# Performance work log

Measured on AMD Instinct MI355X. Metric: run time of the kernel, lower is better.

The kernel has to match this reference:

```python
import jax, jax.numpy as jnp
import numpy as np

B, L, D, H, S, E, FF = 4, 2048, 1024, 16, 512, 8, 4096
DH = D // H  # head dim = 64
EPS = 1e-5


def setup_inputs() -> dict:
    key = jax.random.key(0)
    ks = jax.random.split(key, 12)
    std = 0.02
    return {
        "x": jax.random.normal(ks[0], (B, L, D), jnp.float32),
        "slot_query": jax.random.normal(ks[1], (H, S, DH), jnp.float32) * std,
        "slot_key": jax.random.normal(ks[2], (H, S, DH), jnp.float32) * std,
        "w_dispatch_k": jax.random.normal(ks[3], (D, D), jnp.float32) * std,
        "w_dispatch_v": jax.random.normal(ks[4], (D, D), jnp.float32) * std,
        "w_combine_q": jax.random.normal(ks[5], (D, D), jnp.float32) * std,
        "w_in": jax.random.normal(ks[6], (E, FF, D), jnp.float32) * std,
        "b_in": jnp.zeros((E, FF), jnp.float32),
        "w_out": jax.random.normal(ks[7], (E, D, FF), jnp.float32) * std,
        "b_out": jnp.zeros((E, D), jnp.float32),
        "pre_norm_w": jnp.ones((D,), jnp.float32),
        "pre_norm_b": jnp.zeros((D,), jnp.float32),
    }


def _layer_norm(x, w, b, eps=EPS):
    m = jnp.mean(x, axis=-1, keepdims=True)
    v = jnp.mean(jnp.square(x - m), axis=-1, keepdims=True)
    return (x - m) * jax.lax.rsqrt(v + eps) * w + b


def _sdpa(q, k, v):
    # q: (..., Q, d), k: (..., K, d), v: (..., K, d)
    scale = 1.0 / np.sqrt(q.shape[-1])
    scores = jnp.einsum("...qd,...kd->...qk", q, k) * scale
    p = jax.nn.softmax(scores, axis=-1)
    return jnp.einsum("...qk,...kd->...qd", p, v)


def _split_heads(t):  # (B, N, D) -> (B, H, N, DH)
    b, n, _ = t.shape
    return t.reshape(b, n, H, DH).transpose(0, 2, 1, 3)


def _merge_heads(t):  # (B, H, N, DH) -> (B, N, D)
    b, h, n, d = t.shape
    return t.transpose(0, 2, 1, 3).reshape(b, n, h * d)


def reference(x, slot_query, slot_key, w_dispatch_k, w_dispatch_v, w_combine_q,
              w_in, b_in, w_out, b_out, pre_norm_w, pre_norm_b):
    # pre-norm
    xn = _layer_norm(x, pre_norm_w, pre_norm_b)

    # ---- dispatch: slots attend to tokens ----
    k = _split_heads(xn @ w_dispatch_k.T)        # (B,H,L,DH)
    v = _split_heads(xn @ w_dispatch_v.T)        # (B,H,L,DH)
    y = _sdpa(slot_query[None], k, v)            # (B,H,S,DH)
    y = _merge_heads(y)                          # (B,S,D)

    # ---- experts: batched per-expert MLP with relu^2 activation ----
    y = y.reshape(B, E, S // E, D)
    h = jnp.einsum("besd,efd->besf", y, w_in) + b_in[None, :, None, :]
    h = jnp.square(jax.nn.relu(h))               # relu2
    eo = jnp.einsum("besf,edf->besd", h, w_out) + b_out[None, :, None, :]
    eo = eo.reshape(B, S, D)

    # ---- combine: tokens attend to slots ----
    q = _split_heads(xn @ w_combine_q.T)         # (B,H,L,DH)
    vc = _split_heads(eo)                        # (B,H,S,DH)
    o = _sdpa(q, slot_key[None], vc)             # (B,H,L,DH)
    return _merge_heads(o)                       # (B,L,D)
```

## Files before the change

### kernel.cpp

```cpp
#include <hip/hip_runtime.h>
#include <hip/hip_bf16.h>

#define B_  4
#define L_  2048
#define D_  1024
#define H_  16
#define S_  512
#define E_  8
#define FF_ 4096
#define DH_ 64

typedef _Float16 half8 __attribute__((ext_vector_type(8)));
typedef _Float16 half4v __attribute__((ext_vector_type(4)));
typedef float floatx4 __attribute__((ext_vector_type(4)));
typedef unsigned short u16;

__device__ inline u16 f2h(float v) {
  _Float16 x = (_Float16)v;
  return __builtin_bit_cast(u16, x);
}

__device__ inline void gload_lds16(const void* g, void* l) {
  __builtin_amdgcn_global_load_lds(
      (const __attribute__((address_space(1))) void*)g,
      (__attribute__((address_space(3))) void*)l, 16, 0, 0);
}

__device__ inline int swz(int row, int colh) {
  return row * 64 + (colh ^ ((row & 7) << 3));
}
__device__ inline int swz1(int row, int colh) {
  return row * 64 + ((colh & ~7) ^ ((row & 7) << 3)) + (colh & 7);
}

__global__ __launch_bounds__(256) void ln_f16(const float* __restrict__ x,
    const float* __restrict__ w, const float* __restrict__ bb,
    u16* __restrict__ xn) {
  int row = blockIdx.x;
  int tid = threadIdx.x;
  float4 v = ((const float4*)(x + (long)row * D_))[tid];
  float s = v.x + v.y + v.z + v.w;
  __shared__ float red[4];
  #pragma unroll
  for (int off = 32; off > 0; off >>= 1) s += __shfl_down(s, off);
  int wid = tid >> 6, lane = tid & 63;
  if (lane == 0) red[wid] = s;
  __syncthreads();
  float mean = (red[0] + red[1] + red[2] + red[3]) * (1.0f / D_);
  __syncthreads();
  float dx = v.x - mean, dy = v.y - mean, dz = v.z - mean, dw = v.w - mean;
  float s2 = dx*dx + dy*dy + dz*dz + dw*dw;
  #pragma unroll
  for (int off = 32; off > 0; off >>= 1) s2 += __shfl_down(s2, off);
  if (lane == 0) red[wid] = s2;
  __syncthreads();
  float var = (red[0] + red[1] + red[2] + red[3]) * (1.0f / D_);
  float rstd = rsqrtf(var + 1e-5f);
  float4 wv = ((const float4*)w)[tid];
  float4 bv = ((const float4*)bb)[tid];
  half4v o = { (_Float16)(dx * rstd * wv.x + bv.x),
               (_Float16)(dy * rstd * wv.y + bv.y),
               (_Float16)(dz * rstd * wv.z + bv.z),
               (_Float16)(dw * rstd * wv.w + bv.w) };
  *(half4v*)&xn[(long)row * D_ + tid * 4] = o;
}

__global__ __launch_bounds__(256) void wcvt(const float* __restrict__ w0,
    const float* __restrict__ w1, const float* __restrict__ w2,
    const float* __restrict__ sq, const float* __restrict__ skq,
    u16* __restrict__ dst) {
  long i = ((long)blockIdx.x * 256 + threadIdx.x) * 8;
  const float* src; long off; float sc = 1.0f;
  if (i < 3145728) {
    int wsel = (int)(i >> 20);
    src = (wsel == 0) ? w0 : (wsel == 1) ? w1 : w2;
    off = i & 1048575;
  } else if (i < 3670016) {
    src = sq; off = i - 3145728; sc = 0.125f;
  } else {
    src = skq; off = i - 3670016;
  }
  float4 a = *(const float4*)(src + off);
  float4 b = *(const float4*)(src + off + 4);
  half8 h = { (_Float16)(a.x*sc), (_Float16)(a.y*sc), (_Float16)(a.z*sc), (_Float16)(a.w*sc),
              (_Float16)(b.x*sc), (_Float16)(b.y*sc), (_Float16)(b.z*sc), (_Float16)(b.w*sc) };
  *(half8*)(dst + i) = h;
}

__global__ __launch_bounds__(256) void proj_f16(
    const u16* __restrict__ A, const u16* __restrict__ Wc,
    u16* __restrict__ kh, u16* __restrict__ vT, u16* __restrict__ qh) {
  const int wsel = blockIdx.x >> 3;
  const int n0 = (blockIdx.x & 7) * 128, m0 = blockIdx.y * 128;
  const u16* Bh = Wc + (long)wsel * 1048576;
  const int tid = threadIdx.x, l = tid & 63, w = tid >> 6;
  const int wr = w >> 1, wc = w & 1;
  __shared__ __align__(16) u16 As[3][128 * 32];
  __shared__ __align__(16) u16 Bs[3][128 * 32];
  floatx4 acc[4][4] = {};

  const int ck = (l & 3) ^ ((l >> 3) & 3);
  const long gaA0 = (long)(m0 + w * 32 + (l >> 2)) * D_ + ck * 8;
  const long gaA1 = gaA0 + 16 * D_;
  const long gaB0 = (long)(n0 + w * 32 + (l >> 2)) * D_ + ck * 8;
  const long gaB1 = gaB0 + 16 * D_;

  #define PSTAGE(buf, kt)                                          \
    do {                                                           \
      gload_lds16(A + gaA0 + (kt), &As[buf][(w * 32) * 32]);       \
      gload_lds16(A + gaA1 + (kt), &As[buf][(w * 32 + 16) * 32]);  \
      gload_lds16(Bh + gaB0 + (kt), &Bs[buf][(w * 32) * 32]);      \
      gload_lds16(Bh + gaB1 + (kt), &Bs[buf][(w * 32 + 16) * 32]); \
    } while (0)

  PSTAGE(0, 0);
  PSTAGE(1, 32);

  int c0 = 0, c1 = 1, c2 = 2;
  const int q = l >> 4;
  for (int t = 0; t < 32; ++t) {
    if (t < 31) asm volatile("s_waitcnt vmcnt(4)" ::: "memory");
    else        asm volatile("s_waitcnt vmcnt(0)" ::: "memory");
    __builtin_amdgcn_s_barrier();
    if (t + 2 < 32) PSTAGE(c2, (t + 2) * 32);

    half8 af[4], bfr[4];
    #pragma unroll
    for (int fr = 0; fr < 4; ++fr) {
      int row = wr * 64 + fr * 16 + (l & 15);
      af[fr] = *(const half8*)&As[c0][row * 32 + ((q ^ ((row >> 1) & 3)) << 3)];
    }
    #pragma unroll
    for (int fc = 0; fc < 4; ++fc) {
      int rr = wc * 64 + fc * 16 + (l & 15);
      bfr[fc] = *(const half8*)&Bs[c0][rr * 32 + ((q ^ ((rr >> 1) & 3)) << 3)];
    }
    #pragma unroll
    for (int fr = 0; fr < 4; ++fr)
      #pragma unroll
      for (int fc = 0; fc < 4; ++fc)
        acc[fr][fc] = __builtin_amdgcn_mfma_f32_16x16x32_f16(af[fr], bfr[fc], acc[fr][fc], 0, 0, 0);

    int tmp = c0; c0 = c1; c1 = c2; c2 = tmp;
  }
  #undef PSTAGE

  if (wsel == 1) {
    #pragma unroll
    for (int fr = 0; fr < 4; ++fr)
      #pragma unroll
      for (int fc = 0; fc < 4; ++fc) {
        int row = m0 + wr * 64 + fr * 16 + (l >> 4) * 4;
        int col = n0 + wc * 64 + fc * 16 + (l & 15);
        half4v o = { (_Float16)acc[fr][fc][0], (_Float16)acc[fr][fc][1],
                     (_Float16)acc[fr][fc][2], (_Float16)acc[fr][fc][3] };
        long idx = ((long)(row >> 11) * 1024 + col) * 2048 + (row & 2047);
        *(half4v*)&vT[idx] = o;
      }
  } else {
    u16* C = (wsel == 0) ? kh : qh;
    const float sc = (wsel == 2) ? 0.125f : 1.0f;
    #pragma unroll
    for (int fr = 0; fr < 4; ++fr)
      #pragma unroll
      for (int fc = 0; fc < 4; ++fc)
        #pragma unroll
        for (int r = 0; r < 4; ++r) {
          int row = m0 + wr * 64 + fr * 16 + (l >> 4) * 4 + r;
          int col = n0 + wc * 64 + fc * 16 + (l & 15);
          C[(long)row * D_ + col] = f2h(acc[fr][fc][r] * sc);
        }
  }
}

template<int MODE>
__global__ __launch_bounds__(512) void expert_gemm(
    const u16* __restrict__ A, const float* __restrict__ Bw,
    const float* __restrict__ bias, u16* __restrict__ Ch,
    float* __restrict__ Cp) {
  constexpr int LDA = (MODE == 1) ? D_ : FF_;
  constexpr int LDB = (MODE == 1) ? D_ : FF_;
  const int e = blockIdx.z;
  const int n0 = blockIdx.x * 64;
  const int kc0 = (MODE == 2) ? blockIdx.y * 1024 : 0;
  const int tid = threadIdx.x, l = tid & 63, w = tid >> 6;
  const int wm = w >> 1, wn = w & 1;
  const int lr = l & 15, q = l >> 4;

  __shared__ __align__(16) u16  As[3][256 * 32];
  __shared__ __align__(16) float Bs[3][64 * 32];

  long asrc[2];
  #pragma unroll
  for (int i = 0; i < 2; ++i) {
    int ar = w * 32 + i * 16 + (l >> 2);
    long grow = (MODE == 1) ? ((long)(ar >> 6) * 512 + e * 64 + (ar & 63))
                            : (((long)(ar >> 6) * 8 + e) * 64 + (ar & 63));
    int ck = (l & 3) ^ (ar & 3);
    asrc[i] = grow * (long)LDA + kc0 + ck * 8;
  }
  const float* Bp = Bw + (long)e * (D_ * FF_);
  int brow = w * 8 + (l >> 3);
  int bck = (l & 7) ^ (brow & 7);
  long bsrc = (long)(n0 + brow) * LDB + kc0 + bck * 4;

  floatx4 acc[4][2] = {};

  #define STAGE(buf, kt)                                                 \
    do {                                                                 \
      gload_lds16(A + asrc[0] + (kt), &As[buf][(w * 32) * 32]);          \
      gload_lds16(A + asrc[1] + (kt), &As[buf][(w * 32 + 16) * 32]);     \
      gload_lds16(Bp + bsrc + (kt), &Bs[buf][(w * 8) * 32]);             \
    } while (0)

  STAGE(0, 0);
  STAGE(1, 32);

  int c0 = 0, c1 = 1, c2 = 2;
  for (int t = 0; t < 32; ++t) {
    if (t < 31) asm volatile("s_waitcnt vmcnt(3)" ::: "memory");
    else        asm volatile("s_waitcnt vmcnt(0)" ::: "memory");
    __builtin_amdgcn_s_barrier();
    if (t + 2 < 32) STAGE(c2, (t + 2) * 32);

    half8 af[4];
    #pragma unroll
    for (int fr = 0; fr < 4; ++fr) {
      int row = wm * 64 + fr * 16 + lr;
      af[fr] = *(const half8*)&As[c0][row * 32 + ((q ^ (row & 3)) << 3)];
    }
    half8 bf[2];
    #pragma unroll
    for (int fc = 0; fc < 2; ++fc) {
      int rn = wn * 32 + fc * 16 + lr;
      float4 x0 = *(const float4*)&Bs[c0][rn * 32 + (((2 * q) ^ (rn & 7)) << 2)];
      float4 x1 = *(const float4*)&Bs[c0][rn * 32 + (((2 * q + 1) ^ (rn & 7)) << 2)];
      bf[fc] = (half8){ (_Float16)x0.x, (_Float16)x0.y, (_Float16)x0.z, (_Float16)x0.w,
                        (_Float16)x1.x, (_Float16)x1.y, (_Float16)x1.z, (_Float16)x1.w };
    }
    #pragma unroll
    for (int fr = 0; fr < 4; ++fr)
      #pragma unroll
      for (int fc = 0; fc < 2; ++fc)
        acc[fr][fc] = __builtin_amdgcn_mfma_f32_16x16x32_f16(af[fr], bf[fc], acc[fr][fc], 0, 0, 0);

    int tmp = c0; c0 = c1; c1 = c2; c2 = tmp;
  }
  #undef STAGE

  #pragma unroll
  for (int fr = 0; fr < 4; ++fr)
    #pragma unroll
    for (int fc = 0; fc < 2; ++fc)
      #pragma unroll
      for (int r = 0; r < 4; ++r) {
        int ar = wm * 64 + fr * 16 + q * 4 + r;
        int col = n0 + wn * 32 + fc * 16 + lr;
        float val = acc[fr][fc][r];
        if constexpr (MODE == 1) {
          val += bias[e * FF_ + col];
          val = fmaxf(val, 0.f);
          val *= val;
          Ch[(((long)(ar >> 6) * 8 + e) * 64 + (ar & 63)) * FF_ + col] = f2h(val);
        } else {
          Cp[(((long)blockIdx.y * 8 + e) * 256 + ar) * 1024 + col] = val;
        }
      }
}

__global__ __launch_bounds__(256) void eo_reduce(const float* __restrict__ pb,
    const float* __restrict__ b_out, u16* __restrict__ eoT) {
  long j4 = (long)blockIdx.x * 256 + threadIdx.x;
  long j = j4 * 4;
  float4 s = ((const float4*)pb)[j4];
  #pragma unroll
  for (int c = 1; c < 4; ++c) {
    float4 t = ((const float4*)(pb + (long)c * 2097152))[j4];
    s.x += t.x; s.y += t.y; s.z += t.z; s.w += t.w;
  }
  int e = (int)(j >> 18);
  int rem = (int)(j & 262143);
  int row = rem >> 10, col = rem & 1023;
  float4 bv = *(const float4*)(b_out + e * 1024 + col);
  s.x += bv.x; s.y += bv.y; s.z += bv.z; s.w += bv.w;
  int b = row >> 6;
  int slot = e * 64 + (row & 63);
  float sv[4] = { s.x, s.y, s.z, s.w };
  #pragma unroll
  for (int i = 0; i < 4; ++i) {
    long idx = ((long)b * 1024 + col + i) * 512 + slot;
    eoT[idx] = f2h(sv[i]);
  }
}

template<bool OF32>
__global__ __launch_bounds__(256) void flash_f16(
    const u16* __restrict__ Qg, long qB, long qH, long qR,
    const u16* __restrict__ Kg, long kB, long kH, long kR,
    const u16* __restrict__ VTg, long vB, long vH, long vR,
    void* __restrict__ Og, long oB, long oH, long oR,
    float* __restrict__ pd, float* __restrict__ pacc,
    int Nq, int Nk, int nC) {
  __shared__ __align__(16) u16 Ks[64 * 64];
  __shared__ __align__(16) u16 Vt[64 * 64];
  const int tid = threadIdx.x, l = tid & 63, w = tid >> 6;
  const int g = l >> 4, lq = l & 15;
  const int bh = blockIdx.z, b = bh >> 4, hd = bh & 15;
  const int q0 = blockIdx.x * 64 + w * 16;
  const int chunk = Nk / nC, k0 = blockIdx.y * chunk;

  half8 qf[2];
  #pragma unroll
  for (int ks = 0; ks < 2; ++ks)
    qf[ks] = *(const half8*)(Qg + b * qB + hd * qH +
                             (long)(q0 + lq) * qR + ks * 32 + g * 8);

  const int srow = l >> 3;
  const int scol = ((l & 7) ^ srow) * 8;
  const long kbase = b * kB + hd * kH;
  const long vbase = b * vB + hd * vH;

  float lrun = 0.f;
  floatx4 o[4] = {};

  for (int t = 0; t < chunk; t += 64) {
    #pragma unroll
    for (int i = 0; i < 2; ++i) {
      int u = i * 4 + w;
      gload_lds16(Kg + kbase + (long)(k0 + t + u * 8 + srow) * kR + scol,
                  &Ks[u * 8 * 64]);
      gload_lds16(VTg + vbase + (long)(u * 8 + srow) * vR + k0 + t + scol,
                  &Vt[u * 8 * 64]);
    }
    __syncthreads();

    floatx4 s[4];
    #pragma unroll
    for (int j = 0; j < 4; ++j) s[j] = (floatx4){0.f, 0.f, 0.f, 0.f};
    #pragma unroll
    for (int ks = 0; ks < 2; ++ks)
      #pragma unroll
      for (int j = 0; j < 4; ++j) {
        half8 kf = *(const half8*)&Ks[swz(j * 16 + lq, ks * 32 + g * 8)];
        s[j] = __builtin_amdgcn_mfma_f32_16x16x32_f16(kf, qf[ks], s[j], 0, 0, 0);
      }

    half4v pa[4];
    float rs = 0.f;
    #pragma unroll
    for (int j = 0; j < 4; ++j)
      #pragma unroll
      for (int r = 0; r < 4; ++r) {
        float p = __expf(s[j][r]);
        rs += p;
        pa[j][r] = (_Float16)p;
      }
    lrun += rs;

    #pragma unroll
    for (int j = 0; j < 4; ++j)
      #pragma unroll
      for (int n = 0; n < 4; ++n) {
        half4v vf = *(const half4v*)&Vt[swz1(n * 16 + lq, j * 16 + g * 4)];
        o[n] = __builtin_amdgcn_mfma_f32_16x16x16f16(pa[j], vf, o[n], 0, 0, 0);
      }
    __syncthreads();
  }

  lrun += __shfl_xor(lrun, 16);
  lrun += __shfl_xor(lrun, 32);

  if (nC == 1) {
    float inv = 1.0f / lrun;
    float invr[4];
    #pragma unroll
    for (int r = 0; r < 4; ++r) invr[r] = __shfl(inv, g * 4 + r);
    #pragma unroll
    for (int n = 0; n < 4; ++n)
      #pragma unroll
      for (int r = 0; r < 4; ++r) {
        int row = q0 + g * 4 + r;
        int dh = n * 16 + lq;
        float val = o[n][r] * invr[r];
        long off = b * oB + hd * oH + (long)row * oR + dh;
        if (OF32) ((float*)Og)[off] = val;
        else      ((u16*)Og)[off] = f2h(val);
      }
  } else {
    if (l < 16) pd[((long)bh * Nq + q0 + l) * nC + blockIdx.y] = lrun;
    #pragma unroll
    for (int r = 0; r < 4; ++r) {
      int row = q0 + g * 4 + r;
      long idx = ((long)bh * Nq + row) * nC + blockIdx.y;
      #pragma unroll
      for (int n = 0; n < 4; ++n)
        pacc[idx * 64 + n * 16 + lq] = o[n][r];
    }
  }
}

__global__ __launch_bounds__(256) void finalize_f16(
    const float* __restrict__ pd, const float* __restrict__ pacc,
    u16* __restrict__ outp, int nC, int Nq, long oB, long oH, long oR) {
  int tid = threadIdx.x;
  int row = blockIdx.x * 4 + (tid >> 6);
  int lane = tid & 63;
  long base = (long)row * nC;
  float Dn = 0.f, a = 0.f;
  for (int c = 0; c < nC; ++c) {
    Dn += pd[base + c];
    a += pacc[(base + c) * 64 + lane];
  }
  int bh = row / Nq, qrow = row - bh * Nq;
  int b = bh >> 4, h = bh & 15;
  outp[(long)b * oB + (long)h * oH + (long)qrow * oR + lane] = f2h(a / Dn);
}

extern "C" void kernel_launch(void* const* d_in, const int* in_sizes, int n_in,
                              void* d_out, int out_size, void* d_ws, size_t ws_size,
                              hipStream_t stream) {
  const float* x     = (const float*)d_in[0];
  const float* sq    = (const float*)d_in[1];
  const float* skq   = (const float*)d_in[2];
  const float* wk    = (const float*)d_in[3];
  const float* wv    = (const float*)d_in[4];
  const float* wq    = (const float*)d_in[5];
  const float* w_in  = (const float*)d_in[6];
  const float* b_in  = (const float*)d_in[7];
  const float* w_out = (const float*)d_in[8];
  const float* b_out = (const float*)d_in[9];
  const float* pnw   = (const float*)d_in[10];
  const float* pnb   = (const float*)d_in[11];
  float* out = (float*)d_out;

  u16* ws   = (u16*)d_ws;
  u16* xnh  = ws;
  u16* kh   = xnh + 8388608;
  u16* vTh  = kh  + 8388608;
  u16* qh   = vTh + 8388608;
  u16* yh   = qh  + 8388608;
  u16* hh   = yh  + 2097152;
  u16* eoTh = hh  + 8388608;
  u16* wch  = eoTh + 2097152;
  u16* sqh  = wch + 3145728;
  u16* skh  = wch + 3670016;
  float* pbuf = (float*)(wch + 4194304);
  float* pdb  = pbuf + 8388608;
  float* pacc = pbuf;

  ln_f16<<<8192, 256, 0, stream>>>(x, pnw, pnb, xnh);
  wcvt<<<2048, 256, 0, stream>>>(wk, wv, wq, sq, skq, wch);

  proj_f16<<<dim3(24, 64, 1), 256, 0, stream>>>(xnh, wch, kh, vTh, qh);

  flash_f16<false><<<dim3(8, 2, 64), 256, 0, stream>>>(
      sqh, 0L, (long)(S_ * DH_), (long)DH_,
      kh, (long)(L_ * D_), (long)DH_, (long)D_,
      vTh, (long)(L_ * D_), (long)(DH_ * L_), (long)L_,
      nullptr, 0L, 0L, 0L,
      pdb, pacc, S_, L_, 2);
  finalize_f16<<<8192, 256, 0, stream>>>(pdb, pacc, yh, 2, S_,
      (long)(S_ * D_), (long)DH_, (long)D_);

  expert_gemm<1><<<dim3(64, 1, 8), 512, 0, stream>>>(yh, w_in, b_in, hh, nullptr);
  expert_gemm<2><<<dim3(16, 4, 8), 512, 0, stream>>>(hh, w_out, nullptr, nullptr, pbuf);
  eo_reduce<<<2048, 256, 0, stream>>>(pbuf, b_out, eoTh);

  flash_f16<true><<<dim3(32, 1, 64), 256, 0, stream>>>(
      qh, (long)(L_ * D_), (long)DH_, (long)D_,
      skh, 0L, (long)(S_ * DH_), (long)DH_,
      eoTh, (long)(S_ * D_), (long)(DH_ * S_), (long)S_,
      out, (long)(L_ * D_), (long)DH_, (long)D_,
      nullptr, nullptr, L_, S_, 1);
}
```

Before: 316.8 us.

## Fuse layernorm with weight conversion and simplify projection GEMM pipeline

Merges the layernorm and weight fp32-to-fp16 conversion kernels into one launch, with extra blocks handling the conversion. The projection GEMM drops from a 3-stage pipeline with manual vmcnt waits to a double-buffered loop using __syncthreads, and swaps the grid axes so consecutive blocks walk along M for a fixed weight tile. The aim is to save a launch and improve weight-tile reuse in L2, at the cost of less load/compute overlap in the GEMM.

```diff
diff --git a/kernel.cpp b/kernel.cpp
--- a/kernel.cpp
+++ b/kernel.cpp
@@ -33,11 +33,33 @@
   return row * 64 + ((colh & ~7) ^ ((row & 7) << 3)) + (colh & 7);
 }
 
-__global__ __launch_bounds__(256) void ln_f16(const float* __restrict__ x,
+__global__ __launch_bounds__(256) void ln_wcvt(const float* __restrict__ x,
     const float* __restrict__ w, const float* __restrict__ bb,
-    u16* __restrict__ xn) {
+    u16* __restrict__ xn,
+    const float* __restrict__ w0, const float* __restrict__ w1,
+    const float* __restrict__ w2, const float* __restrict__ sq,
+    const float* __restrict__ skq, u16* __restrict__ dst) {
+  int tid = threadIdx.x;
+  if (blockIdx.x >= 8192) {
+    long i = ((long)(blockIdx.x - 8192) * 256 + tid) * 8;
+    const float* src; long off; float sc = 1.0f;
+    if (i < 3145728) {
+      int wsel = (int)(i >> 20);
+      src = (wsel == 0) ? w0 : (wsel == 1) ? w1 : w2;
+      off = i & 1048575;
+    } else if (i < 3670016) {
+      src = sq; off = i - 3145728; sc = 0.125f;
+    } else {
+      src = skq; off = i - 3670016;
+    }
+    float4 a = *(const float4*)(src + off);
+    float4 b = *(const float4*)(src + off + 4);
+    half8 h = { (_Float16)(a.x*sc), (_Float16)(a.y*sc), (_Float16)(a.z*sc), (_Float16)(a.w*sc),
+                (_Float16)(b.x*sc), (_Float16)(b.y*sc), (_Float16)(b.z*sc), (_Float16)(b.w*sc) };
+    *(half8*)(dst + i) = h;
+    return;
+  }
   int row = blockIdx.x;
-  int tid = threadIdx.x;
   float4 v = ((const float4*)(x + (long)row * D_))[tid];
   float s = v.x + v.y + v.z + v.w;
   __shared__ float red[4];
@@ -65,38 +87,16 @@
   *(half4v*)&xn[(long)row * D_ + tid * 4] = o;
 }
 
-__global__ __launch_bounds__(256) void wcvt(const float* __restrict__ w0,
-    const float* __restrict__ w1, const float* __restrict__ w2,
-    const float* __restrict__ sq, const float* __restrict__ skq,
-    u16* __restrict__ dst) {
-  long i = ((long)blockIdx.x * 256 + threadIdx.x) * 8;
-  const float* src; long off; float sc = 1.0f;
-  if (i < 3145728) {
-    int wsel = (int)(i >> 20);
-    src = (wsel == 0) ? w0 : (wsel == 1) ? w1 : w2;
-    off = i & 1048575;
-  } else if (i < 3670016) {
-    src = sq; off = i - 3145728; sc = 0.125f;
-  } else {
-    src = skq; off = i - 3670016;
-  }
-  float4 a = *(const float4*)(src + off);
-  float4 b = *(const float4*)(src + off + 4);
-  half8 h = { (_Float16)(a.x*sc), (_Float16)(a.y*sc), (_Float16)(a.z*sc), (_Float16)(a.w*sc),
-              (_Float16)(b.x*sc), (_Float16)(b.y*sc), (_Float16)(b.z*sc), (_Float16)(b.w*sc) };
-  *(half8*)(dst + i) = h;
-}
-
 __global__ __launch_bounds__(256) void proj_f16(
     const u16* __restrict__ A, const u16* __restrict__ Wc,
     u16* __restrict__ kh, u16* __restrict__ vT, u16* __restrict__ qh) {
-  const int wsel = blockIdx.x >> 3;
-  const int n0 = (blockIdx.x & 7) * 128, m0 = blockIdx.y * 128;
+  const int wsel = blockIdx.y >> 3;
+  const int n0 = (blockIdx.y & 7) * 128, m0 = blockIdx.x * 128;
   const u16* Bh = Wc + (long)wsel * 1048576;
   const int tid = threadIdx.x, l = tid & 63, w = tid >> 6;
   const int wr = w >> 1, wc = w & 1;
-  __shared__ __align__(16) u16 As[3][128 * 32];
-  __shared__ __align__(16) u16 Bs[3][128 * 32];
+  __shared__ __align__(16) u16 As[2][128 * 32];
+  __shared__ __align__(16) u16 Bs[2][128 * 32];
   floatx4 acc[4][4] = {};
 
   const int ck = (l & 3) ^ ((l >> 3) & 3);
@@ -114,34 +114,30 @@
     } while (0)
 
   PSTAGE(0, 0);
-  PSTAGE(1, 32);
-
-  int c0 = 0, c1 = 1, c2 = 2;
+  __syncthreads();
+
+  int cur = 0;
   const int q = l >> 4;
   for (int t = 0; t < 32; ++t) {
-    if (t < 31) asm volatile("s_waitcnt vmcnt(4)" ::: "memory");
-    else        asm volatile("s_waitcnt vmcnt(0)" ::: "memory");
-    __builtin_amdgcn_s_barrier();
-    if (t + 2 < 32) PSTAGE(c2, (t + 2) * 32);
-
+    if (t < 31) PSTAGE(cur ^ 1, (t + 1) * 32);
     half8 af[4], bfr[4];
     #pragma unroll
     for (int fr = 0; fr < 4; ++fr) {
       int row = wr * 64 + fr * 16 + (l & 15);
-      af[fr] = *(const half8*)&As[c0][row * 32 + ((q ^ ((row >> 1) & 3)) << 3)];
+      af[fr] = *(const half8*)&As[cur][row * 32 + ((q ^ ((row >> 1) & 3)) << 3)];
     }
     #pragma unroll
     for (int fc = 0; fc < 4; ++fc) {
       int rr = wc * 64 + fc * 16 + (l & 15);
-      bfr[fc] = *(const half8*)&Bs[c0][rr * 32 + ((q ^ ((rr >> 1) & 3)) << 3)];
+      bfr[fc] = *(const half8*)&Bs[cur][rr * 32 + ((q ^ ((rr >> 1) & 3)) << 3)];
     }
     #pragma unroll
     for (int fr = 0; fr < 4; ++fr)
       #pragma unroll
       for (int fc = 0; fc < 4; ++fc)
         acc[fr][fc] = __builtin_amdgcn_mfma_f32_16x16x32_f16(af[fr], bfr[fc], acc[fr][fc], 0, 0, 0);
-
-    int tmp = c0; c0 = c1; c1 = c2; c2 = tmp;
+    __syncthreads();
+    cur ^= 1;
   }
   #undef PSTAGE
 
@@ -448,10 +444,9 @@
   float* pdb  = pbuf + 8388608;
   float* pacc = pbuf;
 
-  ln_f16<<<8192, 256, 0, stream>>>(x, pnw, pnb, xnh);
-  wcvt<<<2048, 256, 0, stream>>>(wk, wv, wq, sq, skq, wch);
-
-  proj_f16<<<dim3(24, 64, 1), 256, 0, stream>>>(xnh, wch, kh, vTh, qh);
+  ln_wcvt<<<10240, 256, 0, stream>>>(x, pnw, pnb, xnh, wk, wv, wq, sq, skq, wch);
+
+  proj_f16<<<dim3(64, 24, 1), 256, 0, stream>>>(xnh, wch, kh, vTh, qh);
 
   flash_f16<false><<<dim3(8, 2, 64), 256, 0, stream>>>(
       sqh, 0L, (long)(S_ * DH_), (long)DH_,
```

After: 310.3 us. 1.02x faster.
